# Kernel tuning notes

Hardware: AMD Instinct MI355X
Metric: run time of the kernel (lower is better)

Reference implementation:

```python
import jax, jax.numpy as jnp
import numpy as np

N_SAMPLES = 2 ** 15          # 32768
STEP = 256                   # transform_step_size
WIN = 2048                   # transform/synthesis window
N_FRAMES = N_SAMPLES // STEP # 128
N_COEFFS = WIN // 2 + 1      # 1025
DILATIONS = (1, 2, 4, 8, 16, 32, 64, 1)


def hann(n):
    return 0.5 - 0.5 * jnp.cos(2.0 * jnp.pi * jnp.arange(n, dtype=jnp.float32) / n)


def transform(audio):
    # audio: (B, 1, N) -> magnitude STFT (B, 1024, 128)
    x = audio[:, 0, :]
    x = jnp.pad(x, ((0, 0), (0, WIN - STEP)))  # pad so n_frames == N_SAMPLES // STEP
    idx = np.arange(N_FRAMES)[:, None] * STEP + np.arange(WIN)[None, :]
    frames = x[:, idx] * hann(WIN)
    spec = jnp.abs(jnp.fft.rfft(frames, norm='ortho'))   # (B, F, 1025)
    return spec[..., : N_COEFFS - 1].transpose(0, 2, 1)  # (B, 1024, F)


def conv1x1(x, w, b):
    # x: (B, I, T), w: (O, I, 1), b: (O,)
    return jnp.einsum('oi,bit->bot', w[:, :, 0], x) + b[None, :, None]


def anticausal_block(x, w, b, dilation):
    # kernel_size=2 anti-causal dilated conv: looks at t and t+dilation (pad future)
    x_fut = jnp.pad(x, ((0, 0), (0, 0), (0, dilation)))[:, :, dilation:]
    y = (jnp.einsum('oi,bit->bot', w[:, :, 0], x)
         + jnp.einsum('oi,bit->bot', w[:, :, 1], x_fut)
         + b[None, :, None])
    y = jax.nn.leaky_relu(y, 0.2)
    y = y + x
    # do_norm: per-example max-norm
    y = y / (jnp.max(jnp.abs(y), axis=(1, 2), keepdims=True) + 1e-8)
    return y


def upsample_with_holes(x, desired_size):
    # zero-stuffing upsample: out[..., ::step] = x
    b, c, t = x.shape
    step = desired_size // t
    out = jnp.zeros((b, c, desired_size), x.dtype)
    return out.at[:, :, ::step].set(x)


def freq_domain_resonance(coeffs):
    # coeffs: (1, C, 1025) in [0, 1); per-frame decay = repeated spectral multiply
    c = jnp.clip(coeffs, 0.0, 0.9999)
    exps = jnp.arange(1, N_FRAMES + 1, dtype=coeffs.dtype)
    mags = c[:, :, None, :] ** exps[None, None, :, None]     # (1, C, F, 1025)
    frames = jnp.fft.irfft(mags, n=WIN) * hann(WIN)
    hop = WIN // 2
    total = hop * (N_FRAMES - 1) + WIN
    idx = np.arange(N_FRAMES)[:, None] * hop + np.arange(WIN)[None, :]
    out = jnp.zeros(frames.shape[:2] + (total,), frames.dtype)
    out = out.at[:, :, idx].add(frames)                      # overlap-add
    return out[..., :N_SAMPLES]                              # (1, C, N)


def fft_convolve(a, b):
    # circular-free conv via zero-padding to 2N, keep first N (matches repo fft_convolve)
    n = a.shape[-1]
    spec = jnp.fft.rfft(a, n=2 * n) * jnp.fft.rfft(b, n=2 * n)
    return jnp.fft.irfft(spec, n=2 * n)[..., :n]


def reference(audio, proj_in_w, proj_in_b, blocks_w, blocks_b,
              proj_sparse_w, proj_sparse_b, proj_dense_w, proj_dense_b, resonances):
    spec = transform(audio)                         # (B, 1024, 128)
    h = conv1x1(spec, proj_in_w, proj_in_b)         # (B, 32, 128)
    acc = jnp.zeros_like(h)
    for i, d in enumerate(DILATIONS):               # fixed 8-block stack
        h = anticausal_block(h, blocks_w[i], blocks_b[i], d)
        acc = acc + h
    x = conv1x1(acc, proj_sparse_w, proj_sparse_b)  # (B, 256, 128)
    sparse = jax.nn.relu(x)
    x = conv1x1(sparse, proj_dense_w, proj_dense_b) # (B, 32, 128)
    x = upsample_with_holes(x, N_SAMPLES)           # (B, 32, 32768)
    res = freq_domain_resonance(resonances)         # (1, 32, 32768), broadcast over B
    y = fft_convolve(x, res)                        # (B, 32, 32768)
    y = jnp.sum(y, axis=1, keepdims=True)           # (B, 1, 32768)
    return y, sparse


def setup_inputs() -> dict:
    key = jax.random.key(0)
    ks = jax.random.split(key, 12)
    u = lambda k, shape: jax.random.uniform(k, shape, jnp.float32, -0.05, 0.05)
    return {
        'audio': jax.random.normal(ks[0], (32, 1, N_SAMPLES), jnp.float32),
        'proj_in_w': u(ks[1], (32, 1024, 1)),
        'proj_in_b': jnp.zeros((32,), jnp.float32),
        'blocks_w': u(ks[2], (8, 32, 32, 2)),
        'blocks_b': jnp.zeros((8, 32), jnp.float32),
        'proj_sparse_w': u(ks[3], (256, 32, 1)),
        'proj_sparse_b': jnp.zeros((256,), jnp.float32),
        'proj_dense_w': u(ks[4], (32, 256, 1)),
        'proj_dense_b': jnp.zeros((32,), jnp.float32),
        'resonances': jax.random.uniform(ks[5], (1, 32, N_COEFFS), jnp.float32, 0.0, 1.0),
    }
```

## Files before the change

kernel.cpp:

```cpp
#include <hip/hip_runtime.h>

#define PI_F 3.14159265358979323846f

typedef short bf16x8 __attribute__((ext_vector_type(8)));
typedef float f32x4 __attribute__((ext_vector_type(4)));

#define MFMA16(acc, a, b) \
  acc = __builtin_amdgcn_mfma_f32_16x16x32_bf16(a, b, acc, 0, 0, 0)

#define WS_SPEC   0u
#define WS_H0     4194304u
#define WS_ACC    4325376u
#define WS_V      4456448u
#define WS_WTIN   4587520u
#define WS_WST    4620288u
#define WS_WDT    4628480u
#define WS_FRAMES 4636672u
#define WS_RES    6733824u

#define BIX(a) ((a) + ((a) >> 4))

#define BFLY(I0, I1, C, S)                                   \
  { float2 u = buf[I0]; float2 w = buf[I1];                  \
    float tr = (C) * w.x - (S) * w.y;                        \
    float ti = (C) * w.y + (S) * w.x;                        \
    buf[I0] = make_float2(u.x + tr, u.y + ti);               \
    buf[I1] = make_float2(u.x - tr, u.y - ti); }

#define CMULV(RX, RY, C, S, W) \
  { RX = (C) * (W).x - (S) * (W).y; RY = (C) * (W).y + (S) * (W).x; }

__device__ __forceinline__ void quad_bfly(float2* buf, int a, int h,
                                          float cs, float ss, float cp, float sp) {
  float2 x0 = buf[BIX(a)],         x1 = buf[BIX(a + h)];
  float2 x2 = buf[BIX(a + 2 * h)], x3 = buf[BIX(a + 3 * h)];
  float t1x = cs * x1.x - ss * x1.y, t1y = cs * x1.y + ss * x1.x;
  float t3x = cs * x3.x - ss * x3.y, t3y = cs * x3.y + ss * x3.x;
  float2 y0 = make_float2(x0.x + t1x, x0.y + t1y);
  float2 y1 = make_float2(x0.x - t1x, x0.y - t1y);
  float2 y2 = make_float2(x2.x + t3x, x2.y + t3y);
  float2 y3 = make_float2(x2.x - t3x, x2.y - t3y);
  float u2x = cp * y2.x - sp * y2.y, u2y = cp * y2.y + sp * y2.x;
  float u3x = sp * y3.x + cp * y3.y, u3y = sp * y3.y - cp * y3.x;
  buf[BIX(a)]         = make_float2(y0.x + u2x, y0.y + u2y);
  buf[BIX(a + 2 * h)] = make_float2(y0.x - u2x, y0.y - u2y);
  buf[BIX(a + h)]     = make_float2(y1.x + u3x, y1.y + u3y);
  buf[BIX(a + 3 * h)] = make_float2(y1.x - u3x, y1.y - u3y);
}

__device__ __forceinline__ void octet_bfly(float2* buf, int a, int h,
                                           float cv, float sv) {
  const float R = 0.7071067811865476f;
  float c1 = cv * cv - sv * sv, s1 = 2.f * cv * sv;
  float c2 = c1 * c1 - s1 * s1, s2 = 2.f * c1 * s1;
  float2 x0 = buf[BIX(a)],         x1 = buf[BIX(a + h)];
  float2 x2 = buf[BIX(a + 2 * h)], x3 = buf[BIX(a + 3 * h)];
  float2 x4 = buf[BIX(a + 4 * h)], x5 = buf[BIX(a + 5 * h)];
  float2 x6 = buf[BIX(a + 6 * h)], x7 = buf[BIX(a + 7 * h)];
  float tx, ty;
  CMULV(tx, ty, c2, s2, x1);
  float2 y0 = make_float2(x0.x + tx, x0.y + ty), y1 = make_float2(x0.x - tx, x0.y - ty);
  CMULV(tx, ty, c2, s2, x3);
  float2 y2 = make_float2(x2.x + tx, x2.y + ty), y3 = make_float2(x2.x - tx, x2.y - ty);
  CMULV(tx, ty, c2, s2, x5);
  float2 y4 = make_float2(x4.x + tx, x4.y + ty), y5 = make_float2(x4.x - tx, x4.y - ty);
  CMULV(tx, ty, c2, s2, x7);
  float2 y6 = make_float2(x6.x + tx, x6.y + ty), y7 = make_float2(x6.x - tx, x6.y - ty);
  CMULV(tx, ty, c1, s1, y2);
  float2 z0 = make_float2(y0.x + tx, y0.y + ty), z2 = make_float2(y0.x - tx, y0.y - ty);
  CMULV(tx, ty, c1, s1, y3);
  float2 z1 = make_float2(y1.x + ty, y1.y - tx), z3 = make_float2(y1.x - ty, y1.y + tx);
  CMULV(tx, ty, c1, s1, y6);
  float2 z4 = make_float2(y4.x + tx, y4.y + ty), z6 = make_float2(y4.x - tx, y4.y - ty);
  CMULV(tx, ty, c1, s1, y7);
  float2 z5 = make_float2(y5.x + ty, y5.y - tx), z7 = make_float2(y5.x - ty, y5.y + tx);
  float ca = R * (cv + sv), sa = R * (sv - cv);
  float cb = sv,            sb = -cv;
  float cc = R * (sv - cv), sc = -R * (cv + sv);
  CMULV(tx, ty, cv, sv, z4);
  buf[BIX(a)]         = make_float2(z0.x + tx, z0.y + ty);
  buf[BIX(a + 4 * h)] = make_float2(z0.x - tx, z0.y - ty);
  CMULV(tx, ty, ca, sa, z5);
  buf[BIX(a + h)]     = make_float2(z1.x + tx, z1.y + ty);
  buf[BIX(a + 5 * h)] = make_float2(z1.x - tx, z1.y - ty);
  CMULV(tx, ty, cb, sb, z6);
  buf[BIX(a + 2 * h)] = make_float2(z2.x + tx, z2.y + ty);
  buf[BIX(a + 6 * h)] = make_float2(z2.x - tx, z2.y - ty);
  CMULV(tx, ty, cc, sc, z7);
  buf[BIX(a + 3 * h)] = make_float2(z3.x + tx, z3.y + ty);
  buf[BIX(a + 7 * h)] = make_float2(z3.x - tx, z3.y - ty);
}

__device__ __forceinline__ void fft2048_stages(float2* buf, int tid) {
  octet_bfly(buf, tid << 3, 1, 1.f, 0.f);
  __syncthreads();
  {
    int j = tid & 7;
    int a = ((tid >> 3) << 6) + j;
    float sv, cv;
    __sincosf(-PI_F / 32.f * (float)j, &sv, &cv);
    octet_bfly(buf, a, 8, cv, sv);
  }
  __syncthreads();
  {
    int j = tid & 63;
    int a = ((tid >> 6) << 9) + j;
    float sv, cv;
    __sincosf(-PI_F / 256.f * (float)j, &sv, &cv);
    octet_bfly(buf, a, 64, cv, sv);
  }
  __syncthreads();
  for (int g = tid; g < 512; g += 256) {
    float sp, cp;
    __sincosf(-PI_F / 1024.f * (float)g, &sp, &cp);
    float c2 = cp * cp - sp * sp, s2 = 2.f * cp * sp;
    quad_bfly(buf, g, 512, c2, s2, cp, sp);
  }
  __syncthreads();
}

__global__ __launch_bounds__(256) void k_fft(const float* __restrict__ audio,
                                             const float* __restrict__ resin,
                                             const float* __restrict__ Win,
                                             const float* __restrict__ Ws,
                                             const float* __restrict__ Wd,
                                             const float* __restrict__ bwIn,
                                             float* __restrict__ spec,
                                             float* __restrict__ frames,
                                             float* __restrict__ WT,
                                             float* __restrict__ WsT,
                                             float* __restrict__ WdT,
                                             short* __restrict__ Whg,
                                             short* __restrict__ Wlg) {
  __shared__ float2 buf[2176];
  int blk = blockIdx.x;

  if (blk >= 2560) {
    int i = (blk - 2560) * 256 + threadIdx.x;
    if (i < 32768) { int o = i >> 10, k = i & 1023; WT[k * 32 + o] = Win[i]; }
    if (i < 8192)  { int o2 = i >> 5, m = i & 31;   WsT[m * 256 + o2] = Ws[i]; }
    if (i < 8192)  { int c = i >> 8, o2 = i & 255;  WdT[o2 * 32 + c] = Wd[i]; }
    if (i < 16384) {
      int w = i & 1, m = (i >> 1) & 31, o = (i >> 6) & 31, s = i >> 11;
      float val = bwIn[i];
      unsigned bits = __float_as_uint(val);
      float rem = val - __uint_as_float(bits & 0xffff0000u);
      int row = (s * 2 + w) * 32 + o;
      Whg[row * 32 + m] = (short)(bits >> 16);
      Wlg[row * 32 + m] = (short)(__float_as_uint(rem) >> 16);
    }
    return;
  }

  if (blk < 2048) {
    int b  = blk >> 6;
    int f0 = (blk & 63) * 2;
    for (int j = threadIdx.x; j < 2048; j += 256) {
      float h = 0.5f - 0.5f * __cosf(0.0030679615757712823f * (float)j);
      int i1 = f0 * 256 + j;
      int i2 = i1 + 256;
      float a1 = (i1 < 32768) ? audio[b * 32768 + i1] : 0.f;
      float a2 = (i2 < 32768) ? audio[b * 32768 + i2] : 0.f;
      buf[BIX(__brev((unsigned)j) >> 21)] = make_float2(a1 * h, a2 * h);
    }
    __syncthreads();
    fft2048_stages(buf, threadIdx.x);
    const float scale = 0.5f * 0.022097086912079608f;
    for (int k = threadIdx.x; k < 1024; k += 256) {
      float2 zk = buf[BIX(k)];
      float2 zn = buf[BIX((2048 - k) & 2047)];
      float f1r = zk.x + zn.x, f1i = zk.y - zn.y;
      float f2r = zk.y + zn.y, f2i = zk.x - zn.x;
      spec[(b * 128 + f0) * 1024 + k]     = sqrtf(f1r * f1r + f1i * f1i) * scale;
      spec[(b * 128 + f0 + 1) * 1024 + k] = sqrtf(f2r * f2r + f2i * f2i) * scale;
    }
  } else {
    int r = blk - 2048;
    int c = r >> 4;
    int g = r & 15;
    float e1 = (float)(2 * g + 1);
    for (int k = threadIdx.x; k < 2048; k += 256) {
      int kk = (k <= 1024) ? k : 2048 - k;
      float cv = resin[c * 1025 + kk];
      cv = fminf(fmaxf(cv, 0.f), 0.9999f);
      float m1 = __powf(cv, e1);
      float m2 = m1 * cv;
      buf[BIX(__brev((unsigned)k) >> 21)] = make_float2(m1, m2);
    }
    __syncthreads();
    fft2048_stages(buf, threadIdx.x);
    for (int j = threadIdx.x; j < 2048; j += 256) {
      float h  = 0.5f - 0.5f * __cosf(0.0030679615757712823f * (float)j);
      float sc = h * (1.f / 2048.f);
      float2 z = buf[BIX(j)];
      frames[(c * 32 + 2 * g) * 2048 + j]     = z.x * sc;
      frames[(c * 32 + 2 * g + 1) * 2048 + j] = z.y * sc;
    }
  }
}

__global__ __launch_bounds__(256) void k_proj_in(const float* __restrict__ spec,
                                                 const float* __restrict__ Win,
                                                 const float* __restrict__ bias,
                                                 float* __restrict__ h0) {
  __shared__ float specL[8][1024];
  __shared__ float red[32][8][8];
  int b  = blockIdx.x >> 4;
  int t0 = (blockIdx.x & 15) * 8;
  for (int i = threadIdx.x; i < 8192; i += 256) {
    int tt = i >> 10, k = i & 1023;
    specL[tt][k] = spec[(b * 128 + t0 + tt) * 1024 + k];
  }
  __syncthreads();
  int o = threadIdx.x & 31, p = threadIdx.x >> 5;
  float part[8] = {0.f,0.f,0.f,0.f,0.f,0.f,0.f,0.f};
  const float4* Wrow = (const float4*)(Win + o * 1024);
  for (int k4 = p * 32; k4 < p * 32 + 32; ++k4) {
    float4 w4 = Wrow[k4];
    int k = k4 * 4;
#pragma unroll
    for (int tt = 0; tt < 8; ++tt) {
      float4 s4 = *(const float4*)&specL[tt][k];
      part[tt] += w4.x * s4.x + w4.y * s4.y + w4.z * s4.z + w4.w * s4.w;
    }
  }
#pragma unroll
  for (int tt = 0; tt < 8; ++tt) red[o][tt][p] = part[tt];
  __syncthreads();
  int oo = threadIdx.x >> 3, tt2 = threadIdx.x & 7;
  float s = bias[oo];
#pragma unroll
  for (int p2 = 0; p2 < 8; ++p2) s += red[oo][tt2][p2];
  h0[b * 4096 + oo * 128 + t0 + tt2] = s;
}

__global__ __launch_bounds__(256) void k_obpack(const float* __restrict__ frames,
                                                short* __restrict__ Bh,
                                                short* __restrict__ Bl) {
  int c = blockIdx.x >> 4, o = blockIdx.x & 15;
  int r = threadIdx.x;
  bf16x8 hv, lv;
#pragma unroll
  for (int j = 0; j < 8; ++j) {
    int fo = 8 * o + j;
    int g  = fo >> 2;
    int j0 = ((fo & 3) << 8) + r;
    float val = frames[(c * 32 + g) * 2048 + j0];
    if (g > 0) val += frames[(c * 32 + g - 1) * 2048 + j0 + 1024];
    unsigned bits = __float_as_uint(val);
    float rem = val - __uint_as_float(bits & 0xffff0000u);
    hv[j] = (short)(bits >> 16);
    lv[j] = (short)(__float_as_uint(rem) >> 16);
  }
  int unit = (blockIdx.x * 16 + (r >> 4)) * 16 + (r & 15);
  ((bf16x8*)Bh)[unit] = hv;
  ((bf16x8*)Bl)[unit] = lv;
}

__global__ __launch_bounds__(1024) void k_chain(const float* __restrict__ h0,
                                                const short* __restrict__ Whg,
                                                const short* __restrict__ Wlg,
                                                const float* __restrict__ bb,
                                                float* __restrict__ accout) {
  __shared__ __align__(16) short Hh[192 * 40];
  __shared__ __align__(16) short Hl[192 * 40];
  __shared__ float Hf[128 * 33];
  __shared__ float bL[256];
  __shared__ float red[16];
  int b = blockIdx.x, tid = threadIdx.x;

  for (int i = tid; i < 4096; i += 1024) {
    int t = i & 127;
    int o = i >> 7;
    float val = h0[b * 4096 + i];
    Hf[t * 33 + o] = val;
    unsigned bits = __float_as_uint(val);
    float rem = val - __uint_as_float(bits & 0xffff0000u);
    Hh[t * 40 + o] = (short)(bits >> 16);
    Hl[t * 40 + o] = (short)(__float_as_uint(rem) >> 16);
  }
  for (int i = tid; i < 64 * 40; i += 1024) {
    Hh[128 * 40 + i] = 0;
    Hl[128 * 40 + i] = 0;
  }
  if (tid < 256) bL[tid] = bb[tid];
  __syncthreads();

  int wave = tid >> 6, lane = tid & 63;
  int quad = lane >> 4, l15 = lane & 15;
  int t0 = (wave & 7) * 16, o0 = (wave >> 3) * 16;
  int tD = t0 + quad * 4;
  int oD = o0 + l15;

  const bf16x8* Hh8 = (const bf16x8*)Hh;
  const bf16x8* Hl8 = (const bf16x8*)Hl;
  const bf16x8* Wh8 = (const bf16x8*)Whg;
  const bf16x8* Wl8 = (const bf16x8*)Wlg;

  float accsum[4] = {0.f, 0.f, 0.f, 0.f};
  const int DIL[8] = {1, 2, 4, 8, 16, 32, 64, 1};

#pragma unroll
  for (int s = 0; s < 8; ++s) {
    int arow = t0 + l15;
    int frow = arow + DIL[s];
    bf16x8 Ah = Hh8[arow * 5 + quad];
    bf16x8 Al = Hl8[arow * 5 + quad];
    bf16x8 Fh = Hh8[frow * 5 + quad];
    bf16x8 Fl = Hl8[frow * 5 + quad];
    int w0row = ((s * 2 + 0) * 32 + oD) * 4 + quad;
    int w1row = ((s * 2 + 1) * 32 + oD) * 4 + quad;
    bf16x8 B0h = Wh8[w0row], B0l = Wl8[w0row];
    bf16x8 B1h = Wh8[w1row], B1l = Wl8[w1row];
    float bias = bL[s * 32 + oD];
    f32x4 acc = {bias, bias, bias, bias};
    MFMA16(acc, Ah, B0h); MFMA16(acc, Ah, B0l); MFMA16(acc, Al, B0h);
    MFMA16(acc, Fh, B1h); MFMA16(acc, Fh, B1l); MFMA16(acc, Fl, B1h);
    float hnew[4], lmax = 0.f;
#pragma unroll
    for (int r = 0; r < 4; ++r) {
      float sv = acc[r];
      sv = (sv > 0.f) ? sv : 0.2f * sv;
      sv += Hf[(tD + r) * 33 + oD];
      hnew[r] = sv;
      lmax = fmaxf(lmax, fabsf(sv));
    }
#pragma unroll
    for (int off = 32; off > 0; off >>= 1)
      lmax = fmaxf(lmax, __shfl_down(lmax, off, 64));
    if (lane == 0) red[wave] = lmax;
    __syncthreads();
    float mx = red[0];
#pragma unroll
    for (int i = 1; i < 16; ++i) mx = fmaxf(mx, red[i]);
    float nm = 1.f / (mx + 1e-8f);
#pragma unroll
    for (int r = 0; r < 4; ++r) {
      float hv = hnew[r] * nm;
      accsum[r] += hv;
      int t = tD + r;
      Hf[t * 33 + oD] = hv;
      unsigned bits = __float_as_uint(hv);
      float rem = hv - __uint_as_float(bits & 0xffff0000u);
      Hh[t * 40 + oD] = (short)(bits >> 16);
      Hl[t * 40 + oD] = (short)(__float_as_uint(rem) >> 16);
    }
    __syncthreads();
  }
#pragma unroll
  for (int r = 0; r < 4; ++r)
    accout[b * 4096 + (tD + r) * 32 + oD] = accsum[r];
}

__global__ __launch_bounds__(256) void k_sparse_dense(const float* __restrict__ acc,
                                                      const float* __restrict__ WsT,
                                                      const float* __restrict__ bs,
                                                      const float* __restrict__ WdT,
                                                      const float* __restrict__ bd,
                                                      float* __restrict__ out_sparse,
                                                      float* __restrict__ v) {
  __shared__ float accL[4][32];
  __shared__ float sL[4][256];
  __shared__ float red[8][4][32];
  int b = blockIdx.x >> 5, tq = blockIdx.x & 31;
  int t0 = tq * 4;
  int tid = threadIdx.x;
  if (tid < 128)
    accL[tid >> 5][tid & 31] = acc[b * 4096 + (t0 + (tid >> 5)) * 32 + (tid & 31)];
  __syncthreads();
  float bsv = bs[tid];
  float s0 = bsv, s1 = bsv, s2 = bsv, s3 = bsv;
  for (int m = 0; m < 32; ++m) {
    float w = WsT[m * 256 + tid];
    s0 += w * accL[0][m]; s1 += w * accL[1][m];
    s2 += w * accL[2][m]; s3 += w * accL[3][m];
  }
  s0 = fmaxf(s0, 0.f); s1 = fmaxf(s1, 0.f); s2 = fmaxf(s2, 0.f); s3 = fmaxf(s3, 0.f);
  float* os = out_sparse + b * 32768 + tid * 128 + t0;
  os[0] = s0; os[1] = s1; os[2] = s2; os[3] = s3;
  sL[0][tid] = s0; sL[1][tid] = s1; sL[2][tid] = s2; sL[3][tid] = s3;
  __syncthreads();
  int c = tid & 31, p = tid >> 5;
  float p0 = 0.f, p1 = 0.f, p2 = 0.f, p3 = 0.f;
  for (int jj = 0; jj < 32; ++jj) {
    int o2 = p * 32 + jj;
    float w = WdT[o2 * 32 + c];
    p0 += w * sL[0][o2]; p1 += w * sL[1][o2];
    p2 += w * sL[2][o2]; p3 += w * sL[3][o2];
  }
  red[p][0][c] = p0; red[p][1][c] = p1; red[p][2][c] = p2; red[p][3][c] = p3;
  __syncthreads();
  if (tid < 128) {
    int tt = tid >> 5, cc = tid & 31;
    float vv = bd[cc];
#pragma unroll
    for (int p2i = 0; p2i < 8; ++p2i) vv += red[p2i][tt][cc];
    v[b * 4096 + cc * 128 + t0 + tt] = vv;
  }
}

__global__ __launch_bounds__(512, 4) void k_conv(const float* __restrict__ v,
                                                 const short* __restrict__ Bh,
                                                 const short* __restrict__ Bl,
                                                 float* __restrict__ y) {
  __shared__ __align__(16) short AH[32 * 264];
  __shared__ __align__(16) short AL[32 * 264];
  __shared__ float vwin[2][16][48];

  int xcd  = blockIdx.x & 7;
  int slot = blockIdx.x >> 3;
  int e, b;
  if      (slot < 32) { e = xcd;      b = slot; }
  else if (slot < 64) { e = xcd + 8;  b = slot - 32; }
  else                { e = (xcd < 4) ? (xcd + 16) : (xcd + 12);
                        b = (xcd < 4) ? (slot - 64) : (slot - 48); }
  int j, uc;
  if      (e < 2)  { j = 0; uc = e; }
  else if (e < 6)  { j = 1; uc = e - 2; }
  else if (e < 12) { j = 2; uc = e - 6; }
  else             { j = 3; uc = e - 12; }
  int D0 = 32 * j - 16 * uc;

  for (int i = threadIdx.x; i < 1504; i += 512) {
    int ii = i % 47;
    int r  = i / 47;
    int c  = r & 15, ph = r >> 4;
    int d  = D0 - 15 + ii;
    vwin[ph][c][ii] = (d >= 0 && d < 128)
        ? v[b * 4096 + (16 * ph + c) * 128 + d] : 0.f;
  }
  __syncthreads();

  int lane = threadIdx.x & 63, wave = threadIdx.x >> 6;
  int quad = lane >> 4, l15 = lane & 15;
  int cq   = quad >> 1;
  int og   = 2 * uc + (quad & 1);
  int nt0  = wave * 2;

  f32x4 acc00 = (f32x4)0.f, acc01 = (f32x4)0.f;
  f32x4 acc10 = (f32x4)0.f, acc11 = (f32x4)0.f;

  const bf16x8* AH8 = (const bf16x8*)AH;
  const bf16x8* AL8 = (const bf16x8*)AL;
  const bf16x8* Bh8 = (const bf16x8*)Bh;
  const bf16x8* Bl8 = (const bf16x8*)Bl;
  short2* AH2 = (short2*)AH;
  short2* AL2 = (short2*)AL;

  int abase0 = (0 * 16 + l15) * 33 + quad;
  int abase1 = (1 * 16 + l15) * 33 + quad;

  for (int p = 0; p < 2; ++p) {
    for (int i = threadIdx.x; i < 4096; i += 512) {
      int kk2 = i & 127;
      int row = i >> 7;
      int cl  = kk2 >> 3;
      int uu  = (kk2 & 7) * 2;
      int ii  = row - uu + 15;
      float v0 = vwin[p][cl][ii];
      float v1 = vwin[p][cl][ii - 1];
      unsigned w0 = __float_as_uint(v0), w1 = __float_as_uint(v1);
      float r0 = v0 - __uint_as_float(w0 & 0xffff0000u);
      float r1 = v1 - __uint_as_float(w1 & 0xffff0000u);
      int u2 = row * 132 + kk2;
      AH2[u2] = make_short2((short)(w0 >> 16), (short)(w1 >> 16));
      AL2[u2] = make_short2((short)(__float_as_uint(r0) >> 16),
                            (short)(__float_as_uint(r1) >> 16));
    }
    __syncthreads();

#pragma unroll
    for (int ks = 0; ks < 8; ++ks) {
      bf16x8 ah0 = AH8[abase0 + ks * 4];
      bf16x8 al0 = AL8[abase0 + ks * 4];
      bf16x8 ah1 = AH8[abase1 + ks * 4];
      bf16x8 al1 = AL8[abase1 + ks * 4];
      int c   = 16 * p + 2 * ks + cq;
      int bb0 = (c * 16 + og) * 256 + l15;
      bf16x8 bh0 = Bh8[bb0 + nt0 * 16];
      bf16x8 bl0 = Bl8[bb0 + nt0 * 16];
      bf16x8 bh1 = Bh8[bb0 + (nt0 + 1) * 16];
      bf16x8 bl1 = Bl8[bb0 + (nt0 + 1) * 16];
      MFMA16(acc00, ah0, bh0); MFMA16(acc00, ah0, bl0); MFMA16(acc00, al0, bh0);
      MFMA16(acc10, ah1, bh0); MFMA16(acc10, ah1, bl0); MFMA16(acc10, al1, bh0);
      MFMA16(acc01, ah0, bh1); MFMA16(acc01, ah0, bl1); MFMA16(acc01, al0, bh1);
      MFMA16(acc11, ah1, bh1); MFMA16(acc11, ah1, bl1); MFMA16(acc11, al1, bh1);
    }
    __syncthreads();
  }

  {
    float* yb0 = y + b * 32768 + (32 * j + 0 * 16 + quad * 4) * 256 + l15;
    float* yb1 = y + b * 32768 + (32 * j + 1 * 16 + quad * 4) * 256 + l15;
#pragma unroll
    for (int reg = 0; reg < 4; ++reg) {
      atomicAdd(yb0 + reg * 256 + (nt0 + 0) * 16, acc00[reg]);
      atomicAdd(yb0 + reg * 256 + (nt0 + 1) * 16, acc01[reg]);
      atomicAdd(yb1 + reg * 256 + (nt0 + 0) * 16, acc10[reg]);
      atomicAdd(yb1 + reg * 256 + (nt0 + 1) * 16, acc11[reg]);
    }
  }
}

extern "C" void kernel_launch(void* const* d_in, const int* in_sizes, int n_in,
                              void* d_out, int out_size, void* d_ws, size_t ws_size,
                              hipStream_t stream) {
  const float* audio = (const float*)d_in[0];
  const float* Win   = (const float*)d_in[1];
  const float* bin   = (const float*)d_in[2];
  const float* bw    = (const float*)d_in[3];
  const float* bb    = (const float*)d_in[4];
  const float* Ws    = (const float*)d_in[5];
  const float* bs    = (const float*)d_in[6];
  const float* Wd    = (const float*)d_in[7];
  const float* bd    = (const float*)d_in[8];
  const float* reson = (const float*)d_in[9];

  float* out = (float*)d_out;
  float* ws  = (float*)d_ws;

  float* spec   = ws + WS_SPEC;
  float* h0     = ws + WS_H0;
  float* accb   = ws + WS_ACC;
  float* vbuf   = ws + WS_V;
  float* WT     = ws + WS_WTIN;
  float* WsT    = ws + WS_WST;
  float* WdT    = ws + WS_WDT;
  float* frames = ws + WS_FRAMES;
  short* Bh = (short*)(ws + WS_RES);
  short* Bl = (short*)(ws + WS_RES + 524288u);
  short* Whg = (short*)(ws + WS_V);
  short* Wlg = (short*)(ws + WS_V + 8192u);

  hipMemsetAsync(d_out, 0, 1048576u * sizeof(float), stream);

  k_fft<<<2688, 256, 0, stream>>>(audio, reson, Win, Ws, Wd, bw,
                                  spec, frames, WT, WsT, WdT, Whg, Wlg);
  k_obpack<<<512, 256, 0, stream>>>(frames, Bh, Bl);
  k_proj_in<<<512, 256, 0, stream>>>(spec, Win, bin, h0);
  k_chain<<<32, 1024, 0, stream>>>(h0, Whg, Wlg, bb, accb);
  k_sparse_dense<<<1024, 256, 0, stream>>>(accb, WsT, bs, WdT, bd, out + 1048576, vbuf);
  k_conv<<<640, 512, 0, stream>>>(vbuf, Bh, Bl, out);
}
```

Baseline: 177.6 us.

## Fold resonance packing into chain kernel, drop unused transpose, widen sparse-dense tiles

```diff
diff --git a/kernel.cpp b/kernel.cpp
--- a/kernel.cpp
+++ b/kernel.cpp
@@ -137,7 +137,6 @@
 
   if (blk >= 2560) {
     int i = (blk - 2560) * 256 + threadIdx.x;
-    if (i < 32768) { int o = i >> 10, k = i & 1023; WT[k * 32 + o] = Win[i]; }
     if (i < 8192)  { int o2 = i >> 5, m = i & 31;   WsT[m * 256 + o2] = Ws[i]; }
     if (i < 8192)  { int c = i >> 8, o2 = i & 255;  WdT[o2 * 32 + c] = Wd[i]; }
     if (i < 16384) {
@@ -234,41 +233,45 @@
   h0[b * 4096 + oo * 128 + t0 + tt2] = s;
 }
 
-__global__ __launch_bounds__(256) void k_obpack(const float* __restrict__ frames,
-                                                short* __restrict__ Bh,
-                                                short* __restrict__ Bl) {
-  int c = blockIdx.x >> 4, o = blockIdx.x & 15;
-  int r = threadIdx.x;
-  bf16x8 hv, lv;
-#pragma unroll
-  for (int j = 0; j < 8; ++j) {
-    int fo = 8 * o + j;
-    int g  = fo >> 2;
-    int j0 = ((fo & 3) << 8) + r;
-    float val = frames[(c * 32 + g) * 2048 + j0];
-    if (g > 0) val += frames[(c * 32 + g - 1) * 2048 + j0 + 1024];
-    unsigned bits = __float_as_uint(val);
-    float rem = val - __uint_as_float(bits & 0xffff0000u);
-    hv[j] = (short)(bits >> 16);
-    lv[j] = (short)(__float_as_uint(rem) >> 16);
-  }
-  int unit = (blockIdx.x * 16 + (r >> 4)) * 16 + (r & 15);
-  ((bf16x8*)Bh)[unit] = hv;
-  ((bf16x8*)Bl)[unit] = lv;
-}
-
 __global__ __launch_bounds__(1024) void k_chain(const float* __restrict__ h0,
                                                 const short* __restrict__ Whg,
                                                 const short* __restrict__ Wlg,
                                                 const float* __restrict__ bb,
-                                                float* __restrict__ accout) {
+                                                float* __restrict__ accout,
+                                                const float* __restrict__ frames,
+                                                short* __restrict__ Bh,
+                                                short* __restrict__ Bl) {
   __shared__ __align__(16) short Hh[192 * 40];
   __shared__ __align__(16) short Hl[192 * 40];
   __shared__ float Hf[128 * 33];
   __shared__ float bL[256];
   __shared__ float red[16];
-  int b = blockIdx.x, tid = threadIdx.x;
-
+  int blk = blockIdx.x, tid = threadIdx.x;
+
+  if (blk >= 32) {
+    int ubb = (blk - 32) * 4 + (tid >> 8);
+    int r   = tid & 255;
+    int c   = ubb >> 4, o = ubb & 15;
+    bf16x8 hv, lv;
+#pragma unroll
+    for (int j = 0; j < 8; ++j) {
+      int fo = 8 * o + j;
+      int g  = fo >> 2;
+      int j0 = ((fo & 3) << 8) + r;
+      float val = frames[(c * 32 + g) * 2048 + j0];
+      if (g > 0) val += frames[(c * 32 + g - 1) * 2048 + j0 + 1024];
+      unsigned bits = __float_as_uint(val);
+      float rem = val - __uint_as_float(bits & 0xffff0000u);
+      hv[j] = (short)(bits >> 16);
+      lv[j] = (short)(__float_as_uint(rem) >> 16);
+    }
+    int unit = (ubb * 16 + (r >> 4)) * 16 + (r & 15);
+    ((bf16x8*)Bh)[unit] = hv;
+    ((bf16x8*)Bl)[unit] = lv;
+    return;
+  }
+
+  int b = blk;
   for (int i = tid; i < 4096; i += 1024) {
     int t = i & 127;
     int o = i >> 7;
@@ -359,38 +362,43 @@
                                                       const float* __restrict__ bd,
                                                       float* __restrict__ out_sparse,
                                                       float* __restrict__ v) {
-  __shared__ float accL[4][32];
-  __shared__ float sL[4][256];
-  __shared__ float red[8][4][32];
-  int b = blockIdx.x >> 5, tq = blockIdx.x & 31;
-  int t0 = tq * 4;
+  __shared__ float accL[8][32];
+  __shared__ float sL[8][256];
+  __shared__ float red[8][8][32];
+  int b = blockIdx.x >> 4, tq = blockIdx.x & 15;
+  int t0 = tq * 8;
   int tid = threadIdx.x;
-  if (tid < 128)
-    accL[tid >> 5][tid & 31] = acc[b * 4096 + (t0 + (tid >> 5)) * 32 + (tid & 31)];
+  accL[tid >> 5][tid & 31] = acc[b * 4096 + (t0 + (tid >> 5)) * 32 + (tid & 31)];
   __syncthreads();
   float bsv = bs[tid];
-  float s0 = bsv, s1 = bsv, s2 = bsv, s3 = bsv;
+  float s[8];
+#pragma unroll
+  for (int j = 0; j < 8; ++j) s[j] = bsv;
   for (int m = 0; m < 32; ++m) {
     float w = WsT[m * 256 + tid];
-    s0 += w * accL[0][m]; s1 += w * accL[1][m];
-    s2 += w * accL[2][m]; s3 += w * accL[3][m];
-  }
-  s0 = fmaxf(s0, 0.f); s1 = fmaxf(s1, 0.f); s2 = fmaxf(s2, 0.f); s3 = fmaxf(s3, 0.f);
+#pragma unroll
+    for (int j = 0; j < 8; ++j) s[j] += w * accL[j][m];
+  }
   float* os = out_sparse + b * 32768 + tid * 128 + t0;
-  os[0] = s0; os[1] = s1; os[2] = s2; os[3] = s3;
-  sL[0][tid] = s0; sL[1][tid] = s1; sL[2][tid] = s2; sL[3][tid] = s3;
+#pragma unroll
+  for (int j = 0; j < 8; ++j) {
+    s[j] = fmaxf(s[j], 0.f);
+    os[j] = s[j];
+    sL[j][tid] = s[j];
+  }
   __syncthreads();
   int c = tid & 31, p = tid >> 5;
-  float p0 = 0.f, p1 = 0.f, p2 = 0.f, p3 = 0.f;
+  float pp[8] = {0.f,0.f,0.f,0.f,0.f,0.f,0.f,0.f};
   for (int jj = 0; jj < 32; ++jj) {
     int o2 = p * 32 + jj;
     float w = WdT[o2 * 32 + c];
-    p0 += w * sL[0][o2]; p1 += w * sL[1][o2];
-    p2 += w * sL[2][o2]; p3 += w * sL[3][o2];
-  }
-  red[p][0][c] = p0; red[p][1][c] = p1; red[p][2][c] = p2; red[p][3][c] = p3;
-  __syncthreads();
-  if (tid < 128) {
+#pragma unroll
+    for (int j = 0; j < 8; ++j) pp[j] += w * sL[j][o2];
+  }
+#pragma unroll
+  for (int j = 0; j < 8; ++j) red[p][j][c] = pp[j];
+  __syncthreads();
+  {
     int tt = tid >> 5, cc = tid & 31;
     float vv = bd[cc];
 #pragma unroll
@@ -536,9 +544,8 @@
 
   k_fft<<<2688, 256, 0, stream>>>(audio, reson, Win, Ws, Wd, bw,
                                   spec, frames, WT, WsT, WdT, Whg, Wlg);
-  k_obpack<<<512, 256, 0, stream>>>(frames, Bh, Bl);
   k_proj_in<<<512, 256, 0, stream>>>(spec, Win, bin, h0);
-  k_chain<<<32, 1024, 0, stream>>>(h0, Whg, Wlg, bb, accb);
-  k_sparse_dense<<<1024, 256, 0, stream>>>(accb, WsT, bs, WdT, bd, out + 1048576, vbuf);
+  k_chain<<<160, 1024, 0, stream>>>(h0, Whg, Wlg, bb, accb, frames, Bh, Bl);
+  k_sparse_dense<<<512, 256, 0, stream>>>(accb, WsT, bs, WdT, bd, out + 1048576, vbuf);
   k_conv<<<640, 512, 0, stream>>>(vbuf, Bh, Bl, out);
 }
```

After: 174.5 us. No clear change (-1.8%).
